# Kernel tuning notes

Measured on AMD Instinct MI355X. Metric: run time of the kernel, lower is better.

Reference implementation:

```python
import jax, jax.numpy as jnp
import numpy as np

NEG_INF = -1e30


def setup_inputs() -> dict:
    key = jax.random.key(0)
    k1, k2, k3 = jax.random.split(key, 3)
    B, H, HKV, S, D = 2, 16, 4, 2048, 128
    q = jax.random.normal(k1, (B, H, S, D), dtype=jnp.float32)
    k = jax.random.normal(k2, (B, HKV, S, D), dtype=jnp.float32)
    v = jax.random.normal(k3, (B, HKV, S, D), dtype=jnp.float32)
    return {"q": q, "k": k, "v": v}


def reference(q, k, v):
    # Flash attention math (exact, non-tiled reference): causal + sliding-window
    # masked softmax(QK^T * scale) V with GQA head grouping.
    B, H, M, D = q.shape
    _, HKV, N, _ = k.shape
    G = H // HKV  # num_kv_groups
    W = 512       # sliding window size
    scale = 1.0 / jnp.sqrt(jnp.float32(D))

    qg = q.reshape(B, HKV, G, M, D)
    # scores: [B, HKV, G, M, N]
    scores = jnp.einsum("bkgmd,bknd->bkgmn", qg, k) * scale

    i = jnp.arange(M)[:, None]
    j = jnp.arange(N)[None, :]
    # causal: j <= i ; sliding window: only last W keys visible (i - j < W)
    keep = (j <= i) & ((i - j) < W)
    scores = jnp.where(keep[None, None, None], scores, NEG_INF)

    p = jax.nn.softmax(scores.astype(jnp.float32), axis=-1).astype(q.dtype)
    out = jnp.einsum("bkgmn,bknd->bkgmd", p, v)
    return out.reshape(B, H, M, D)
```

## Files before the change

kernel.cpp:

```cpp
#include <hip/hip_runtime.h>
#include <hip/hip_bf16.h>
#include <stdint.h>

#define SEQ 2048
#define HD  128
#define WIN 512
#define NH  16
#define NKV 4
#define BATCH 2

typedef __attribute__((ext_vector_type(8))) short bf16x8;
typedef __attribute__((ext_vector_type(4))) short bf16x4;
typedef __attribute__((ext_vector_type(4))) float f32x4;
typedef __attribute__((ext_vector_type(4))) uint32_t u32x4;
typedef __attribute__((ext_vector_type(2))) uint32_t u32x2;

#define EXP2(x) __builtin_amdgcn_exp2f(x)

#define KSTR 136
#define VSTR 72
#define VT_ROWS (HD * VSTR + (HD / 4) * 4)
__device__ __forceinline__ int vt_off(int row, int col) {
    return row * VSTR + (row >> 2) * 4 + col;
}

__device__ __forceinline__ uint32_t pk2(float a, float b) {
    __hip_bfloat162 h = __float22bfloat162_rn(make_float2(a, b));
    return *reinterpret_cast<uint32_t*>(&h);
}

__global__ __launch_bounds__(512, 2)
void fa_mfma(
    const float* __restrict__ q,
    const float* __restrict__ k,
    const float* __restrict__ v,
    float* __restrict__ out)
{
    const int tid  = threadIdx.x;
    const int wave = tid >> 6;
    const int lane = tid & 63;
    const int l4   = lane >> 4;
    const int l15  = lane & 15;

    const int bh   = blockIdx.x >> 4;
    const int qblk = blockIdx.x & 15;
    const int q0   = qblk << 7;
    const int hkv  = (bh & (NH - 1)) >> 2;
    const int b    = bh >> 4;

    const int i0   = q0 + wave * 16;

    __shared__ __align__(16) uint16_t lds_k[2][64 * KSTR];
    __shared__ __align__(16) uint16_t lds_vt[2][VT_ROWS];

    const float scale2 = 0.08838834764831845f * 1.4426950408889634f;

    const size_t qbase  = (size_t)bh * SEQ * HD;
    const size_t kvbase = (size_t)(b * NKV + hkv) * SEQ * HD;

    bf16x8 qf[4];
    {
        const float* qr = q + qbase + (size_t)(i0 + l15) * HD;
        #pragma unroll
        for (int ks = 0; ks < 4; ++ks) {
            const float4* g = reinterpret_cast<const float4*>(qr + ks * 32 + l4 * 8);
            float4 a = g[0], bq = g[1];
            u32x4 t;
            t.x = pk2(a.x * scale2, a.y * scale2);
            t.y = pk2(a.z * scale2, a.w * scale2);
            t.z = pk2(bq.x * scale2, bq.y * scale2);
            t.w = pk2(bq.z * scale2, bq.w * scale2);
            qf[ks] = __builtin_bit_cast(bf16x8, t);
        }
    }

    f32x4 O[8];
    #pragma unroll
    for (int a2 = 0; a2 < 8; ++a2) O[a2] = (f32x4){0.f, 0.f, 0.f, 0.f};
    float mrow = -1e30f;
    float lrow = 0.f;

    const int kt_lo_blk = (q0 >= 512) ? ((q0 - 511) >> 6) : 0;
    const int kt_hi_blk = (q0 + 127) >> 6;
    const int lo_w = (i0 >= 512) ? ((i0 - 511) >> 6) : 0;
    const int hi_w = (i0 + 15) >> 6;

    const int vdg = tid & 31;
    const int vkg = tid >> 5;
    float4 rKa[2], rKb[2], rV[4];

    auto prefetch_k = [&](int kt) {
        const float* kp = k + kvbase + (size_t)kt * 64 * HD;
        #pragma unroll
        for (int it = 0; it < 2; ++it) {
            int flat8 = tid + it * 512, key = flat8 >> 4, ch = flat8 & 15;
            const float4* g = reinterpret_cast<const float4*>(kp + key * HD + ch * 8);
            rKa[it] = g[0]; rKb[it] = g[1];
        }
    };
    auto prefetch_v = [&](int kt) {
        const float* vp = v + kvbase + (size_t)kt * 64 * HD;
        #pragma unroll
        for (int r = 0; r < 4; ++r)
            rV[r] = *reinterpret_cast<const float4*>(vp + (vkg * 4 + r) * HD + vdg * 4);
    };

    auto pack_k = [&](int pb) {
        #pragma unroll
        for (int it = 0; it < 2; ++it) {
            int flat8 = tid + it * 512, key = flat8 >> 4, ch = flat8 & 15;
            uint4 wv;
            wv.x = pk2(rKa[it].x, rKa[it].y);  wv.y = pk2(rKa[it].z, rKa[it].w);
            wv.z = pk2(rKb[it].x, rKb[it].y);  wv.w = pk2(rKb[it].z, rKb[it].w);
            *reinterpret_cast<uint4*>(&lds_k[pb][key * KSTR + ch * 8]) = wv;
        }
    };
    auto pack_v = [&](int pb) {
        const float* rvf = reinterpret_cast<const float*>(rV);
        #pragma unroll
        for (int i = 0; i < 4; ++i) {
            u32x2 wv;
            wv.x = pk2(rvf[0 * 4 + i], rvf[1 * 4 + i]);
            wv.y = pk2(rvf[2 * 4 + i], rvf[3 * 4 + i]);
            *reinterpret_cast<u32x2*>(&lds_vt[pb][vt_off(vdg * 4 + i, vkg * 4)]) = wv;
        }
    };

    prefetch_k(kt_lo_blk);
    prefetch_v(kt_lo_blk);
    pack_k(0);
    pack_v(0);
    __syncthreads();

    int par = 0;
    for (int kt = kt_lo_blk; kt <= kt_hi_blk; ++kt) {
        const bool more = (kt < kt_hi_blk);
        if (more) prefetch_k(kt + 1);

        if (kt >= lo_w && kt <= hi_w) {
            f32x4 sf[4];
            #pragma unroll
            for (int mt = 0; mt < 4; ++mt) sf[mt] = (f32x4){0.f, 0.f, 0.f, 0.f};
            __builtin_amdgcn_s_setprio(1);
            #pragma unroll
            for (int mt = 0; mt < 4; ++mt) {
                #pragma unroll
                for (int ks = 0; ks < 4; ++ks) {
                    bf16x8 af = *reinterpret_cast<const bf16x8*>(
                        &lds_k[par][(mt * 16 + l15) * KSTR + ks * 32 + l4 * 8]);
                    sf[mt] = __builtin_amdgcn_mfma_f32_16x16x32_bf16(
                        af, qf[ks], sf[mt], 0, 0, 0);
                }
            }
            __builtin_amdgcn_s_setprio(0);
            if (more) { pack_k(par ^ 1); prefetch_v(kt + 1); }
            const bool needmask = (kt == hi_w) || (kt == lo_w && i0 > 511);
            if (needmask) {
                const int iq = i0 + l15;
                #pragma unroll
                for (int mt = 0; mt < 4; ++mt) {
                    int jb = kt * 64 + mt * 16 + l4 * 4;
                    #pragma unroll
                    for (int r = 0; r < 4; ++r) {
                        int j = jb + r;
                        if (!((j <= iq) && (iq - j < WIN))) sf[mt][r] = -1e30f;
                    }
                }
            }
            float a0 = fmaxf(fmaxf(sf[0][0], sf[0][1]), fmaxf(sf[0][2], sf[0][3]));
            float a1 = fmaxf(fmaxf(sf[1][0], sf[1][1]), fmaxf(sf[1][2], sf[1][3]));
            float a2 = fmaxf(fmaxf(sf[2][0], sf[2][1]), fmaxf(sf[2][2], sf[2][3]));
            float a3 = fmaxf(fmaxf(sf[3][0], sf[3][1]), fmaxf(sf[3][2], sf[3][3]));
            float tm = fmaxf(fmaxf(a0, a1), fmaxf(a2, a3));
            tm = fmaxf(tm, __shfl_xor(tm, 16, 64));
            tm = fmaxf(tm, __shfl_xor(tm, 32, 64));
            const bool defer = __all(tm <= mrow + 8.0f);
            if (!defer) {
                float mn = fmaxf(mrow, tm);
                float alpha = EXP2(mrow - mn);
                mrow = mn;
                lrow *= alpha;
                #pragma unroll
                for (int r = 0; r < 4; ++r) {
                    float ar = __shfl(alpha, l4 * 4 + r, 64);
                    #pragma unroll
                    for (int nt = 0; nt < 8; ++nt) O[nt][r] *= ar;
                }
            }
            bf16x4 pfrag[4];
            {
                float me = fmaxf(mrow, -1e20f);
                float s[4];
                #pragma unroll
                for (int mt = 0; mt < 4; ++mt) {
                    float p0 = EXP2(sf[mt][0] - me);
                    float p1 = EXP2(sf[mt][1] - me);
                    float p2 = EXP2(sf[mt][2] - me);
                    float p3 = EXP2(sf[mt][3] - me);
                    u32x2 t;
                    t.x = pk2(p0, p1);
                    t.y = pk2(p2, p3);
                    pfrag[mt] = __builtin_bit_cast(bf16x4, t);
                    s[mt] = (p0 + p1) + (p2 + p3);
                }
                float ts = (s[0] + s[1]) + (s[2] + s[3]);
                ts += __shfl_xor(ts, 16, 64);
                ts += __shfl_xor(ts, 32, 64);
                lrow += ts;
            }
            if (more) pack_v(par ^ 1);
            __builtin_amdgcn_s_setprio(1);
            #pragma unroll
            for (int s = 0; s < 2; ++s) {
                bf16x8 pa = __builtin_shufflevector(pfrag[2 * s], pfrag[2 * s + 1],
                                                    0, 1, 2, 3, 4, 5, 6, 7);
                #pragma unroll
                for (int nt = 0; nt < 8; ++nt) {
                    const int vr = nt * 16 + l15;
                    bf16x4 v0 = *reinterpret_cast<const bf16x4*>(
                        &lds_vt[par][vt_off(vr, s * 32 + l4 * 4)]);
                    bf16x4 v1 = *reinterpret_cast<const bf16x4*>(
                        &lds_vt[par][vt_off(vr, s * 32 + 16 + l4 * 4)]);
                    bf16x8 vf = __builtin_shufflevector(v0, v1, 0, 1, 2, 3, 4, 5, 6, 7);
                    O[nt] = __builtin_amdgcn_mfma_f32_16x16x32_bf16(pa, vf, O[nt], 0, 0, 0);
                }
            }
            __builtin_amdgcn_s_setprio(0);
        } else {
            if (more) { prefetch_v(kt + 1); pack_k(par ^ 1); pack_v(par ^ 1); }
        }
        __syncthreads();
        par ^= 1;
    }

    {
        float inv = 1.0f / lrow;
        #pragma unroll
        for (int r = 0; r < 4; ++r) {
            float li = __shfl(inv, l4 * 4 + r, 64);
            int row = i0 + l4 * 4 + r;
            float* orow = out + qbase + (size_t)row * HD;
            #pragma unroll
            for (int nt = 0; nt < 8; ++nt)
                orow[nt * 16 + l15] = O[nt][r] * li;
        }
    }
}

extern "C" void kernel_launch(void* const* d_in, const int* in_sizes, int n_in,
                              void* d_out, int out_size, void* d_ws, size_t ws_size,
                              hipStream_t stream) {
    const float* q = (const float*)d_in[0];
    const float* k = (const float*)d_in[1];
    const float* v = (const float*)d_in[2];
    float* out     = (float*)d_out;

    hipLaunchKernelGGL(fa_mfma, dim3(BATCH * NH * (SEQ / 128)), dim3(512), 0, stream,
                       q, k, v, out);
}
```

Before: 143.5 us.

## Pre-convert K/V to swizzled bf16 in workspace and stage via global_load_lds

```diff
diff --git a/kernel.cpp b/kernel.cpp
--- a/kernel.cpp
+++ b/kernel.cpp
@@ -17,23 +17,76 @@
 
 #define EXP2(x) __builtin_amdgcn_exp2f(x)
 
-#define KSTR 136
-#define VSTR 72
-#define VT_ROWS (HD * VSTR + (HD / 4) * 4)
-__device__ __forceinline__ int vt_off(int row, int col) {
-    return row * VSTR + (row >> 2) * 4 + col;
-}
+#define AS1(p) ((const __attribute__((address_space(1))) uint32_t*)(p))
+#define AS3(p) ((__attribute__((address_space(3))) uint32_t*)(p))
 
 __device__ __forceinline__ uint32_t pk2(float a, float b) {
     __hip_bfloat162 h = __float22bfloat162_rn(make_float2(a, b));
     return *reinterpret_cast<uint32_t*>(&h);
 }
 
-__global__ __launch_bounds__(512, 2)
-void fa_mfma(
-    const float* __restrict__ q,
+__global__ __launch_bounds__(256) void prep_kv(
     const float* __restrict__ k,
     const float* __restrict__ v,
+    uint16_t* __restrict__ kb,
+    uint16_t* __restrict__ vt)
+{
+    const int tile = blockIdx.x;
+    const int kvh  = tile >> 5;
+    const int kt   = tile & 31;
+    const int t    = threadIdx.x;
+
+    const float* ksrc = k + ((size_t)kvh * SEQ + kt * 64) * HD;
+    const float* vsrc = v + ((size_t)kvh * SEQ + kt * 64) * HD;
+    uint16_t* kdst = kb + ((size_t)kvh * SEQ + kt * 64) * HD;
+    uint16_t* vdst = vt + ((size_t)kvh * 32 + kt) * (size_t)(64 * HD);
+
+    __shared__ uint16_t lv[64][132];
+
+    #pragma unroll
+    for (int i = 0; i < 8; ++i) {
+        int u = t + i * 256;
+        int row = u >> 5, c4 = u & 31;
+        float4 f = *reinterpret_cast<const float4*>(vsrc + row * HD + c4 * 4);
+        u32x2 w; w.x = pk2(f.x, f.y); w.y = pk2(f.z, f.w);
+        *reinterpret_cast<u32x2*>(&lv[row][c4 * 4]) = w;
+    }
+    #pragma unroll
+    for (int i = 0; i < 8; ++i) {
+        int u = t + i * 256;
+        int row = u >> 5, c4 = u & 31;
+        float4 f = *reinterpret_cast<const float4*>(ksrc + row * HD + c4 * 4);
+        u32x2 w; w.x = pk2(f.x, f.y); w.y = pk2(f.z, f.w);
+        int col = c4 * 4;
+        int e = row * HD + ((((col >> 3) ^ (row & 7)) << 3) | (col & 7));
+        *reinterpret_cast<u32x2*>(&kdst[e]) = w;
+    }
+    __syncthreads();
+    #pragma unroll
+    for (int i = 0; i < 4; ++i) {
+        int g = t + i * 256;
+        int dim = g >> 3, pg = g & 7;
+        uint32_t w[4];
+        #pragma unroll
+        for (int jj = 0; jj < 4; ++jj) {
+            int p0 = pg * 8 + jj * 2;
+            int s0 = p0 >> 5, w0 = p0 & 31;
+            int key0 = s0 * 32 + ((w0 >> 2) & 1) * 16 + (w0 >> 3) * 4 + (w0 & 3);
+            int p1 = p0 + 1;
+            int s1 = p1 >> 5, w1 = p1 & 31;
+            int key1 = s1 * 32 + ((w1 >> 2) & 1) * 16 + (w1 >> 3) * 4 + (w1 & 3);
+            w[jj] = (uint32_t)lv[key0][dim] | ((uint32_t)lv[key1][dim] << 16);
+        }
+        int e = dim * 64 + ((pg ^ (dim & 7)) << 3);
+        u32x4 wv = {w[0], w[1], w[2], w[3]};
+        *reinterpret_cast<u32x4*>(&vdst[e]) = wv;
+    }
+}
+
+__global__ __launch_bounds__(512, 2) void fa_mfma(
+    const float* __restrict__ q,
+    const uint16_t* __restrict__ kb,
+    const uint16_t* __restrict__ vt,
     float* __restrict__ out)
 {
     const int tid  = threadIdx.x;
@@ -50,13 +103,14 @@
 
     const int i0   = q0 + wave * 16;
 
-    __shared__ __align__(16) uint16_t lds_k[2][64 * KSTR];
-    __shared__ __align__(16) uint16_t lds_vt[2][VT_ROWS];
+    __shared__ __align__(16) uint16_t lds_k[2][64 * HD];
+    __shared__ __align__(16) uint16_t lds_vt[2][64 * HD];
 
     const float scale2 = 0.08838834764831845f * 1.4426950408889634f;
 
-    const size_t qbase  = (size_t)bh * SEQ * HD;
-    const size_t kvbase = (size_t)(b * NKV + hkv) * SEQ * HD;
+    const size_t qbase = (size_t)bh * SEQ * HD;
+    const uint16_t* kt_base = kb + (size_t)(b * NKV + hkv) * SEQ * HD;
+    const uint16_t* vt_base = vt + (size_t)(b * NKV + hkv) * SEQ * HD;
 
     bf16x8 qf[4];
     {
@@ -85,57 +139,27 @@
     const int lo_w = (i0 >= 512) ? ((i0 - 511) >> 6) : 0;
     const int hi_w = (i0 + 15) >> 6;
 
-    const int vdg = tid & 31;
-    const int vkg = tid >> 5;
-    float4 rKa[2], rKb[2], rV[4];
-
-    auto prefetch_k = [&](int kt) {
-        const float* kp = k + kvbase + (size_t)kt * 64 * HD;
-        #pragma unroll
-        for (int it = 0; it < 2; ++it) {
-            int flat8 = tid + it * 512, key = flat8 >> 4, ch = flat8 & 15;
-            const float4* g = reinterpret_cast<const float4*>(kp + key * HD + ch * 8);
-            rKa[it] = g[0]; rKb[it] = g[1];
+    auto stage = [&](int kt, int pb) {
+        const uint16_t* ks = kt_base + (size_t)kt * 64 * HD;
+        const uint16_t* vs = vt_base + (size_t)kt * 64 * HD;
+        const int ch = wave * 2;
+        #pragma unroll
+        for (int c = 0; c < 2; ++c) {
+            __builtin_amdgcn_global_load_lds(
+                AS1(ks + (ch + c) * 512 + lane * 8),
+                AS3(&lds_k[pb][(ch + c) * 512]), 16, 0, 0);
+            __builtin_amdgcn_global_load_lds(
+                AS1(vs + (ch + c) * 512 + lane * 8),
+                AS3(&lds_vt[pb][(ch + c) * 512]), 16, 0, 0);
         }
     };
-    auto prefetch_v = [&](int kt) {
-        const float* vp = v + kvbase + (size_t)kt * 64 * HD;
-        #pragma unroll
-        for (int r = 0; r < 4; ++r)
-            rV[r] = *reinterpret_cast<const float4*>(vp + (vkg * 4 + r) * HD + vdg * 4);
-    };
-
-    auto pack_k = [&](int pb) {
-        #pragma unroll
-        for (int it = 0; it < 2; ++it) {
-            int flat8 = tid + it * 512, key = flat8 >> 4, ch = flat8 & 15;
-            uint4 wv;
-            wv.x = pk2(rKa[it].x, rKa[it].y);  wv.y = pk2(rKa[it].z, rKa[it].w);
-            wv.z = pk2(rKb[it].x, rKb[it].y);  wv.w = pk2(rKb[it].z, rKb[it].w);
-            *reinterpret_cast<uint4*>(&lds_k[pb][key * KSTR + ch * 8]) = wv;
-        }
-    };
-    auto pack_v = [&](int pb) {
-        const float* rvf = reinterpret_cast<const float*>(rV);
-        #pragma unroll
-        for (int i = 0; i < 4; ++i) {
-            u32x2 wv;
-            wv.x = pk2(rvf[0 * 4 + i], rvf[1 * 4 + i]);
-            wv.y = pk2(rvf[2 * 4 + i], rvf[3 * 4 + i]);
-            *reinterpret_cast<u32x2*>(&lds_vt[pb][vt_off(vdg * 4 + i, vkg * 4)]) = wv;
-        }
-    };
-
-    prefetch_k(kt_lo_blk);
-    prefetch_v(kt_lo_blk);
-    pack_k(0);
-    pack_v(0);
+
+    stage(kt_lo_blk, 0);
     __syncthreads();
 
     int par = 0;
     for (int kt = kt_lo_blk; kt <= kt_hi_blk; ++kt) {
-        const bool more = (kt < kt_hi_blk);
-        if (more) prefetch_k(kt + 1);
+        if (kt < kt_hi_blk) stage(kt + 1, par ^ 1);
 
         if (kt >= lo_w && kt <= hi_w) {
             f32x4 sf[4];
@@ -144,16 +168,16 @@
             __builtin_amdgcn_s_setprio(1);
             #pragma unroll
             for (int mt = 0; mt < 4; ++mt) {
+                const int arow = mt * 16 + l15;
                 #pragma unroll
                 for (int ks = 0; ks < 4; ++ks) {
                     bf16x8 af = *reinterpret_cast<const bf16x8*>(
-                        &lds_k[par][(mt * 16 + l15) * KSTR + ks * 32 + l4 * 8]);
+                        &lds_k[par][arow * HD + ((((ks * 4 + l4) ^ (arow & 7))) << 3)]);
                     sf[mt] = __builtin_amdgcn_mfma_f32_16x16x32_bf16(
                         af, qf[ks], sf[mt], 0, 0, 0);
                 }
             }
             __builtin_amdgcn_s_setprio(0);
-            if (more) { pack_k(par ^ 1); prefetch_v(kt + 1); }
             const bool needmask = (kt == hi_w) || (kt == lo_w && i0 > 511);
             if (needmask) {
                 const int iq = i0 + l15;
@@ -208,6 +232,224 @@
                 ts += __shfl_xor(ts, 32, 64);
                 lrow += ts;
             }
+            __builtin_amdgcn_s_setprio(1);
+            #pragma unroll
+            for (int s = 0; s < 2; ++s) {
+                bf16x8 pa = __builtin_shufflevector(pfrag[2 * s], pfrag[2 * s + 1],
+                                                    0, 1, 2, 3, 4, 5, 6, 7);
+                #pragma unroll
+                for (int nt = 0; nt < 8; ++nt) {
+                    const int vr = nt * 16 + l15;
+                    bf16x8 vf = *reinterpret_cast<const bf16x8*>(
+                        &lds_vt[par][vr * 64 + ((((s * 4 + l4) ^ (vr & 7))) << 3)]);
+                    O[nt] = __builtin_amdgcn_mfma_f32_16x16x32_bf16(pa, vf, O[nt], 0, 0, 0);
+                }
+            }
+            __builtin_amdgcn_s_setprio(0);
+        }
+        __syncthreads();
+        par ^= 1;
+    }
+
+    {
+        float inv = 1.0f / lrow;
+        #pragma unroll
+        for (int r = 0; r < 4; ++r) {
+            float li = __shfl(inv, l4 * 4 + r, 64);
+            int row = i0 + l4 * 4 + r;
+            float* orow = out + qbase + (size_t)row * HD;
+            #pragma unroll
+            for (int nt = 0; nt < 8; ++nt)
+                orow[nt * 16 + l15] = O[nt][r] * li;
+        }
+    }
+}
+
+#define KSTR 136
+#define VSTR 72
+#define VT_ROWS (HD * VSTR + (HD / 4) * 4)
+__device__ __forceinline__ int vt_off(int row, int col) {
+    return row * VSTR + (row >> 2) * 4 + col;
+}
+
+__global__ __launch_bounds__(512, 2)
+void fa_mfma_fused(
+    const float* __restrict__ q,
+    const float* __restrict__ k,
+    const float* __restrict__ v,
+    float* __restrict__ out)
+{
+    const int tid  = threadIdx.x;
+    const int wave = tid >> 6;
+    const int lane = tid & 63;
+    const int l4   = lane >> 4;
+    const int l15  = lane & 15;
+
+    const int bh   = blockIdx.x >> 4;
+    const int qblk = blockIdx.x & 15;
+    const int q0   = qblk << 7;
+    const int hkv  = (bh & (NH - 1)) >> 2;
+    const int b    = bh >> 4;
+
+    const int i0   = q0 + wave * 16;
+
+    __shared__ __align__(16) uint16_t lds_k[2][64 * KSTR];
+    __shared__ __align__(16) uint16_t lds_vt[2][VT_ROWS];
+
+    const float scale2 = 0.08838834764831845f * 1.4426950408889634f;
+
+    const size_t qbase  = (size_t)bh * SEQ * HD;
+    const size_t kvbase = (size_t)(b * NKV + hkv) * SEQ * HD;
+
+    bf16x8 qf[4];
+    {
+        const float* qr = q + qbase + (size_t)(i0 + l15) * HD;
+        #pragma unroll
+        for (int ks = 0; ks < 4; ++ks) {
+            const float4* g = reinterpret_cast<const float4*>(qr + ks * 32 + l4 * 8);
+            float4 a = g[0], bq = g[1];
+            u32x4 t;
+            t.x = pk2(a.x * scale2, a.y * scale2);
+            t.y = pk2(a.z * scale2, a.w * scale2);
+            t.z = pk2(bq.x * scale2, bq.y * scale2);
+            t.w = pk2(bq.z * scale2, bq.w * scale2);
+            qf[ks] = __builtin_bit_cast(bf16x8, t);
+        }
+    }
+
+    f32x4 O[8];
+    #pragma unroll
+    for (int a2 = 0; a2 < 8; ++a2) O[a2] = (f32x4){0.f, 0.f, 0.f, 0.f};
+    float mrow = -1e30f;
+    float lrow = 0.f;
+
+    const int kt_lo_blk = (q0 >= 512) ? ((q0 - 511) >> 6) : 0;
+    const int kt_hi_blk = (q0 + 127) >> 6;
+    const int lo_w = (i0 >= 512) ? ((i0 - 511) >> 6) : 0;
+    const int hi_w = (i0 + 15) >> 6;
+
+    const int vdg = tid & 31;
+    const int vkg = tid >> 5;
+    float4 rKa[2], rKb[2], rV[4];
+
+    auto prefetch_k = [&](int kt) {
+        const float* kp = k + kvbase + (size_t)kt * 64 * HD;
+        #pragma unroll
+        for (int it = 0; it < 2; ++it) {
+            int flat8 = tid + it * 512, key = flat8 >> 4, ch = flat8 & 15;
+            const float4* g = reinterpret_cast<const float4*>(kp + key * HD + ch * 8);
+            rKa[it] = g[0]; rKb[it] = g[1];
+        }
+    };
+    auto prefetch_v = [&](int kt) {
+        const float* vp = v + kvbase + (size_t)kt * 64 * HD;
+        #pragma unroll
+        for (int r = 0; r < 4; ++r)
+            rV[r] = *reinterpret_cast<const float4*>(vp + (vkg * 4 + r) * HD + vdg * 4);
+    };
+    auto pack_k = [&](int pb) {
+        #pragma unroll
+        for (int it = 0; it < 2; ++it) {
+            int flat8 = tid + it * 512, key = flat8 >> 4, ch = flat8 & 15;
+            uint4 wv;
+            wv.x = pk2(rKa[it].x, rKa[it].y);  wv.y = pk2(rKa[it].z, rKa[it].w);
+            wv.z = pk2(rKb[it].x, rKb[it].y);  wv.w = pk2(rKb[it].z, rKb[it].w);
+            *reinterpret_cast<uint4*>(&lds_k[pb][key * KSTR + ch * 8]) = wv;
+        }
+    };
+    auto pack_v = [&](int pb) {
+        const float* rvf = reinterpret_cast<const float*>(rV);
+        #pragma unroll
+        for (int i = 0; i < 4; ++i) {
+            u32x2 wv;
+            wv.x = pk2(rvf[0 * 4 + i], rvf[1 * 4 + i]);
+            wv.y = pk2(rvf[2 * 4 + i], rvf[3 * 4 + i]);
+            *reinterpret_cast<u32x2*>(&lds_vt[pb][vt_off(vdg * 4 + i, vkg * 4)]) = wv;
+        }
+    };
+
+    prefetch_k(kt_lo_blk);
+    prefetch_v(kt_lo_blk);
+    pack_k(0);
+    pack_v(0);
+    __syncthreads();
+
+    int par = 0;
+    for (int kt = kt_lo_blk; kt <= kt_hi_blk; ++kt) {
+        const bool more = (kt < kt_hi_blk);
+        if (more) prefetch_k(kt + 1);
+
+        if (kt >= lo_w && kt <= hi_w) {
+            f32x4 sf[4];
+            #pragma unroll
+            for (int mt = 0; mt < 4; ++mt) sf[mt] = (f32x4){0.f, 0.f, 0.f, 0.f};
+            __builtin_amdgcn_s_setprio(1);
+            #pragma unroll
+            for (int mt = 0; mt < 4; ++mt) {
+                #pragma unroll
+                for (int ks = 0; ks < 4; ++ks) {
+                    bf16x8 af = *reinterpret_cast<const bf16x8*>(
+                        &lds_k[par][(mt * 16 + l15) * KSTR + ks * 32 + l4 * 8]);
+                    sf[mt] = __builtin_amdgcn_mfma_f32_16x16x32_bf16(
+                        af, qf[ks], sf[mt], 0, 0, 0);
+                }
+            }
+            __builtin_amdgcn_s_setprio(0);
+            if (more) { pack_k(par ^ 1); prefetch_v(kt + 1); }
+            const bool needmask = (kt == hi_w) || (kt == lo_w && i0 > 511);
+            if (needmask) {
+                const int iq = i0 + l15;
+                #pragma unroll
+                for (int mt = 0; mt < 4; ++mt) {
+                    int jb = kt * 64 + mt * 16 + l4 * 4;
+                    #pragma unroll
+                    for (int r = 0; r < 4; ++r) {
+                        int j = jb + r;
+                        if (!((j <= iq) && (iq - j < WIN))) sf[mt][r] = -1e30f;
+                    }
+                }
+            }
+            float a0 = fmaxf(fmaxf(sf[0][0], sf[0][1]), fmaxf(sf[0][2], sf[0][3]));
+            float a1 = fmaxf(fmaxf(sf[1][0], sf[1][1]), fmaxf(sf[1][2], sf[1][3]));
+            float a2 = fmaxf(fmaxf(sf[2][0], sf[2][1]), fmaxf(sf[2][2], sf[2][3]));
+            float a3 = fmaxf(fmaxf(sf[3][0], sf[3][1]), fmaxf(sf[3][2], sf[3][3]));
+            float tm = fmaxf(fmaxf(a0, a1), fmaxf(a2, a3));
+            tm = fmaxf(tm, __shfl_xor(tm, 16, 64));
+            tm = fmaxf(tm, __shfl_xor(tm, 32, 64));
+            const bool defer = __all(tm <= mrow + 8.0f);
+            if (!defer) {
+                float mn = fmaxf(mrow, tm);
+                float alpha = EXP2(mrow - mn);
+                mrow = mn;
+                lrow *= alpha;
+                #pragma unroll
+                for (int r = 0; r < 4; ++r) {
+                    float ar = __shfl(alpha, l4 * 4 + r, 64);
+                    #pragma unroll
+                    for (int nt = 0; nt < 8; ++nt) O[nt][r] *= ar;
+                }
+            }
+            bf16x4 pfrag[4];
+            {
+                float me = fmaxf(mrow, -1e20f);
+                float s[4];
+                #pragma unroll
+                for (int mt = 0; mt < 4; ++mt) {
+                    float p0 = EXP2(sf[mt][0] - me);
+                    float p1 = EXP2(sf[mt][1] - me);
+                    float p2 = EXP2(sf[mt][2] - me);
+                    float p3 = EXP2(sf[mt][3] - me);
+                    u32x2 t;
+                    t.x = pk2(p0, p1);
+                    t.y = pk2(p2, p3);
+                    pfrag[mt] = __builtin_bit_cast(bf16x4, t);
+                    s[mt] = (p0 + p1) + (p2 + p3);
+                }
+                float ts = (s[0] + s[1]) + (s[2] + s[3]);
+                ts += __shfl_xor(ts, 16, 64);
+                ts += __shfl_xor(ts, 32, 64);
+                lrow += ts;
+            }
             if (more) pack_v(par ^ 1);
             __builtin_amdgcn_s_setprio(1);
             #pragma unroll
@@ -255,6 +497,18 @@
     const float* v = (const float*)d_in[2];
     float* out     = (float*)d_out;
 
-    hipLaunchKernelGGL(fa_mfma, dim3(BATCH * NH * (SEQ / 128)), dim3(512), 0, stream,
-                       q, k, v, out);
+    const size_t kv_elems = (size_t)BATCH * NKV * SEQ * HD;
+    const size_t ws_needed = kv_elems * 2u * sizeof(uint16_t);
+
+    if (d_ws != nullptr && ws_size >= ws_needed) {
+        uint16_t* kb  = (uint16_t*)d_ws;
+        uint16_t* vtw = kb + kv_elems;
+        hipLaunchKernelGGL(prep_kv, dim3(BATCH * NKV * (SEQ / 64)), dim3(256), 0,
+                           stream, k, v, kb, vtw);
+        hipLaunchKernelGGL(fa_mfma, dim3(BATCH * NH * (SEQ / 128)), dim3(512), 0,
+                           stream, q, kb, vtw, out);
+    } else {
+        hipLaunchKernelGGL(fa_mfma_fused, dim3(BATCH * NH * (SEQ / 128)), dim3(512),
+                           0, stream, q, k, v, out);
+    }
 }
```

Result: faster. 121.0 us (-15.7%).
